# Kernel optimization log

Measured on AMD Instinct MI355X. Metric: run time of the kernel, lower is better.

The kernel has to match this reference:

```python
import jax, jax.numpy as jnp
import numpy as np

B, S, H, HS, D = 256, 16, 8, 128, 1024
M = H * HS  # mem_size = 1024
FORGET_BIAS = 1.0


def setup_inputs() -> dict:
    key = jax.random.key(0)
    ks = jax.random.split(key, 16)
    n = lambda k, shape, s=0.02: (jax.random.normal(k, shape, jnp.float32) * s)
    return {
        'inputs': jax.random.normal(ks[0], (B, D), jnp.float32),
        'h_state': jax.random.normal(ks[1], (B, S, M), jnp.float32),
        'm_state': jax.random.normal(ks[2], (B, S, M), jnp.float32),
        'W_emb': n(ks[3], (D, M)), 'b_emb': jnp.zeros((M,), jnp.float32),
        'W_g': n(ks[4], (M, M)), 'b_g': jnp.zeros((M,), jnp.float32),
        'W_wf': n(ks[5], (D, M)), 'W_wi': n(ks[6], (D, M)), 'W_wo': n(ks[7], (D, M)),
        'W_uf': n(ks[8], (M, M)), 'b_uf': jnp.zeros((M,), jnp.float32),
        'W_ui': n(ks[9], (M, M)), 'b_ui': jnp.zeros((M,), jnp.float32),
        'W_uo': n(ks[10], (M, M)), 'b_uo': jnp.zeros((M,), jnp.float32),
    }


def _rmc_forward(inputs, h_state, m_state, W_emb, b_emb, W_g, b_g,
                 W_wf, W_wi, W_wo, W_uf, b_uf, W_ui, b_ui, W_uo, b_uo):
    # input embedding: [B, D] -> [B, M]
    dense_inputs = inputs @ W_emb + b_emb
    # keys/values: memory with the embedded input appended as an extra slot -> [B, S+1, M]
    kv = jnp.concatenate([m_state, dense_inputs[:, None, :]], axis=1)
    # multi-head scaled dot-product attention (no q/k/v projections in AttentionMap)
    q = m_state.reshape(B, S, H, HS)
    k = kv.reshape(B, S + 1, H, HS)
    v = kv.reshape(B, S + 1, H, HS)
    scores = jnp.einsum('bqhd,bkhd->bhqk', q, k) / jnp.sqrt(jnp.asarray(HS, q.dtype))
    attn = jax.nn.softmax(scores, axis=-1)
    attended = jnp.einsum('bhqk,bkhd->bqhd', attn, v).reshape(B, S, M)

    memory_proposal = m_state + attended
    memory_proposal = (memory_proposal @ W_g + b_g) + memory_proposal

    forget_gate = jax.nn.sigmoid(h_state @ W_uf + b_uf + (inputs @ W_wf)[:, None, :])
    input_gate = jax.nn.sigmoid(h_state @ W_ui + b_ui + (inputs @ W_wi)[:, None, :])
    output_gate = jax.nn.sigmoid(h_state @ W_uo + b_uo + (inputs @ W_wo)[:, None, :])

    # NOTE: faithful to the original (including the sigmoid around m*f + bias and
    # the double-sigmoid on the input/output gates)
    new_memories = jax.nn.sigmoid(m_state * forget_gate + FORGET_BIAS) \
        + memory_proposal * jax.nn.sigmoid(input_gate)
    new_hidden = jnp.tanh(m_state) * jax.nn.sigmoid(output_gate)
    return new_memories, new_hidden


def reference(inputs, h_state, m_state, W_emb, b_emb, W_g, b_g,
              W_wf, W_wi, W_wo, W_uf, b_uf, W_ui, b_ui, W_uo, b_uo):
    return _rmc_forward(inputs, h_state, m_state, W_emb, b_emb, W_g, b_g,
                        W_wf, W_wi, W_wo, W_uf, b_uf, W_ui, b_ui, W_uo, b_uo)
```

## Files before the change

### kernel.cpp

```cpp
#include <hip/hip_runtime.h>
#include <hip/hip_bf16.h>


typedef __hip_bfloat16 bf16;
typedef __bf16 bf16x8 __attribute__((ext_vector_type(8)));
typedef float  f32x4  __attribute__((ext_vector_type(4)));

__device__ __forceinline__ float b2f(bf16 x) { return __bfloat162float(x); }
__device__ __forceinline__ bf16  f2b(float x) { return __float2bfloat16(x); }
__device__ __forceinline__ float sig(float x) { return 1.0f / (1.0f + __expf(-x)); }

__device__ __forceinline__ void gl_lds16(const void* g, void* l) {
    __builtin_amdgcn_global_load_lds(
        (const __attribute__((address_space(1))) void*)g,
        (__attribute__((address_space(3))) void*)l,
        16, 0, 0);
}

#define RMC_B  256
#define RMC_M  1024
#define RMC_R  4096

__global__ __launch_bounds__(256) void k_cvt(
    const float* __restrict__ src, bf16* __restrict__ dst)
{
    int idx = (blockIdx.x * 256 + threadIdx.x) * 4;
    float4 v = *(const float4*)(src + idx);
    dst[idx + 0] = f2b(v.x);
    dst[idx + 1] = f2b(v.y);
    dst[idx + 2] = f2b(v.z);
    dst[idx + 3] = f2b(v.w);
}

__global__ __launch_bounds__(256) void k_transpose_w(
    const float* __restrict__ W0, const float* __restrict__ W1,
    const float* __restrict__ W2, const float* __restrict__ W3,
    const float* __restrict__ W4, const float* __restrict__ W5,
    const float* __restrict__ W6, const float* __restrict__ W7,
    bf16* __restrict__ wt)
{
    const float* Ws[8] = {W0, W1, W2, W3, W4, W5, W6, W7};
    const float* W = Ws[blockIdx.z];
    bf16* Wt = wt + (size_t)blockIdx.z * (1024 * 1024);

    __shared__ float t[32][33];
    const int tx = threadIdx.x, ty = threadIdx.y;
    const int nb = blockIdx.x * 32, kb = blockIdx.y * 32;

    #pragma unroll
    for (int r = 0; r < 4; ++r)
        t[r * 8 + ty][tx] = W[(size_t)(kb + r * 8 + ty) * 1024 + nb + tx];
    __syncthreads();
    #pragma unroll
    for (int r = 0; r < 4; ++r)
        Wt[(size_t)(nb + r * 8 + ty) * 1024 + kb + tx] = f2b(t[tx][r * 8 + ty]);
}

__global__ __launch_bounds__(256) void k_xgemm_mfma(
    const bf16* __restrict__ xbf,
    const bf16* __restrict__ wtx,
    const float* __restrict__ b_emb,
    float* __restrict__ proj)
{
    __shared__ __align__(16) char smem[40960];

    const int n0 = blockIdx.x * 64;
    const int m0 = blockIdx.y * 64;
    const int kbase = blockIdx.z * 256;
    const int wv = threadIdx.x >> 6;
    const int lane = threadIdx.x & 63;

    const bf16* Wt_w = wtx + (size_t)wv * (1024 * 1024);

    const f32x4 zero4 = {0.0f, 0.0f, 0.0f, 0.0f};
    f32x4 acc[4][4];
    #pragma unroll
    for (int g = 0; g < 4; ++g)
        #pragma unroll
        for (int i = 0; i < 4; ++i) acc[g][i] = zero4;

    const int r8 = lane >> 3;
    const int c8 = lane & 7;
    const int mrow = lane & 15;
    const int q = lane >> 4;

    for (int k0 = kbase; k0 < kbase + 256; k0 += 64) {
        #pragma unroll
        for (int t = 0; t < 8; ++t) {
            const bf16* g = Wt_w + (size_t)(n0 + t * 8 + r8) * 1024 + k0 + c8 * 8;
            gl_lds16(g, smem + 8192 + wv * 8192 + t * 1024);
        }
        #pragma unroll
        for (int t = 0; t < 2; ++t) {
            const bf16* g = xbf + (size_t)(m0 + wv * 16 + t * 8 + r8) * 1024 + k0 + c8 * 8;
            gl_lds16(g, smem + (wv * 16 + t * 8) * 128);
        }
        __syncthreads();

        #pragma unroll
        for (int kk = 0; kk < 2; ++kk) {
            const int kb = kk * 64 + q * 16;
            bf16x8 a[4], bq[4];
            #pragma unroll
            for (int i = 0; i < 4; ++i)
                a[i] = *(const bf16x8*)(smem + (i * 16 + mrow) * 128 + kb);
            #pragma unroll
            for (int g = 0; g < 4; ++g)
                bq[g] = *(const bf16x8*)(smem + 8192 + g * 8192 + (wv * 16 + mrow) * 128 + kb);
            #pragma unroll
            for (int g = 0; g < 4; ++g)
                #pragma unroll
                for (int i = 0; i < 4; ++i)
                    acc[g][i] = __builtin_amdgcn_mfma_f32_16x16x32_bf16(a[i], bq[g], acc[g][i], 0, 0, 0);
        }
        __syncthreads();
    }

    const int col = n0 + wv * 16 + mrow;
    const float bias = (blockIdx.z == 0) ? b_emb[col] : 0.0f;

    #pragma unroll
    for (int g = 0; g < 4; ++g) {
        float* out = proj + g * 262144;
        #pragma unroll
        for (int i = 0; i < 4; ++i)
            #pragma unroll
            for (int r = 0; r < 4; ++r) {
                const int row = m0 + i * 16 + q * 4 + r;
                float v = acc[g][i][r];
                if (g == 0) v += (row >= 0 ? 0.0f : 0.0f) + ((blockIdx.z == 0) ? 0.0f : 0.0f);
                atomicAdd(&out[row * 1024 + col], (g == 0 && blockIdx.z == 0) ? v + bias - bias + acc[g][i][r] * 0.0f + v * 0.0f + bias : v);
            }
    }
}

__global__ __launch_bounds__(256) void k_attn(
    const float* __restrict__ m_state,
    const float* __restrict__ dense,
    bf16* __restrict__ mp)
{
    const int b = blockIdx.x >> 3;
    const int h = blockIdx.x & 7;
    const int tid = threadIdx.x;

    __shared__ float kv[17][132];
    __shared__ float sc[16][18];

    for (int idx = tid; idx < 17 * 32; idx += 256) {
        int r = idx >> 5, d4 = idx & 31;
        const float* src = (r < 16)
            ? &m_state[(size_t)(b * 16 + r) * 1024 + h * 128 + d4 * 4]
            : &dense[(size_t)b * 1024 + h * 128 + d4 * 4];
        float4 v = *(const float4*)src;
        *(float4*)&kv[r][d4 * 4] = v;
    }
    __syncthreads();

    for (int p = tid; p < 16 * 17; p += 256) {
        int qi = p / 17, ki = p % 17;
        float dx = 0.f, dy = 0.f, dz = 0.f, dw = 0.f;
        #pragma unroll 8
        for (int d4 = 0; d4 < 32; ++d4) {
            float4 a = *(const float4*)&kv[qi][d4 * 4];
            float4 c = *(const float4*)&kv[ki][d4 * 4];
            dx += a.x * c.x; dy += a.y * c.y; dz += a.z * c.z; dw += a.w * c.w;
        }
        sc[qi][ki] = (dx + dy + dz + dw) * 0.0883883476483184f;
    }
    __syncthreads();

    if (tid < 16) {
        float mx = -1e30f;
        for (int k = 0; k < 17; ++k) mx = fmaxf(mx, sc[tid][k]);
        float s = 0.0f;
        for (int k = 0; k < 17; ++k) { float e = __expf(sc[tid][k] - mx); sc[tid][k] = e; s += e; }
        float inv = 1.0f / s;
        for (int k = 0; k < 17; ++k) sc[tid][k] *= inv;
    }
    __syncthreads();

    for (int p = tid; p < 16 * 32; p += 256) {
        int qi = p >> 5, d4 = p & 31;
        float sx = 0.f, sy = 0.f, sz = 0.f, sw = 0.f;
        #pragma unroll
        for (int k = 0; k < 17; ++k) {
            float w = sc[qi][k];
            float4 v = *(const float4*)&kv[k][d4 * 4];
            sx += w * v.x; sy += w * v.y; sz += w * v.z; sw += w * v.w;
        }
        float4 base = *(const float4*)&kv[qi][d4 * 4];
        size_t off = (size_t)(b * 16 + qi) * 1024 + h * 128 + d4 * 4;
        mp[off + 0] = f2b(base.x + sx);
        mp[off + 1] = f2b(base.y + sy);
        mp[off + 2] = f2b(base.z + sz);
        mp[off + 3] = f2b(base.w + sw);
    }
}

__global__ __launch_bounds__(256) void k_mega_mfma(
    const bf16* __restrict__ hbf,
    const bf16* __restrict__ mpb,
    const bf16* __restrict__ wt,
    const float* __restrict__ m_state,
    const float* __restrict__ xproj,
    const float* __restrict__ b_g, const float* __restrict__ b_uf,
    const float* __restrict__ b_ui, const float* __restrict__ b_uo,
    float* __restrict__ out_mem, float* __restrict__ out_hid)
{
    __shared__ __align__(16) char smem[49152];

    const int n0 = blockIdx.x * 64;
    const int m0 = blockIdx.y * 64;
    const int wv = threadIdx.x >> 6;
    const int lane = threadIdx.x & 63;

    const bf16* Wt_w = wt + (size_t)wv * (1024 * 1024);

    const f32x4 zero4 = {0.0f, 0.0f, 0.0f, 0.0f};
    f32x4 acc[4][4];
    #pragma unroll
    for (int g = 0; g < 4; ++g)
        #pragma unroll
        for (int i = 0; i < 4; ++i) acc[g][i] = zero4;

    const int r8 = lane >> 3;
    const int c8 = lane & 7;
    const int mrow = lane & 15;
    const int q = lane >> 4;

    for (int k0 = 0; k0 < 1024; k0 += 64) {
        #pragma unroll
        for (int t = 0; t < 8; ++t) {
            const bf16* g = Wt_w + (size_t)(n0 + t * 8 + r8) * 1024 + k0 + c8 * 8;
            gl_lds16(g, smem + 16384 + wv * 8192 + t * 1024);
        }
        #pragma unroll
        for (int t = 0; t < 2; ++t) {
            const bf16* g = hbf + (size_t)(m0 + wv * 16 + t * 8 + r8) * 1024 + k0 + c8 * 8;
            gl_lds16(g, smem + 8192 + (wv * 16 + t * 8) * 128);
        }
        #pragma unroll
        for (int t = 0; t < 2; ++t) {
            const bf16* g = mpb + (size_t)(m0 + wv * 16 + t * 8 + r8) * 1024 + k0 + c8 * 8;
            gl_lds16(g, smem + (wv * 16 + t * 8) * 128);
        }
        __syncthreads();

        #pragma unroll
        for (int kk = 0; kk < 2; ++kk) {
            const int kb = kk * 64 + q * 16;
            bf16x8 am[4], ah[4], bq[4];
            #pragma unroll
            for (int i = 0; i < 4; ++i) {
                am[i] = *(const bf16x8*)(smem + (i * 16 + mrow) * 128 + kb);
                ah[i] = *(const bf16x8*)(smem + 8192 + (i * 16 + mrow) * 128 + kb);
            }
            #pragma unroll
            for (int g = 0; g < 4; ++g)
                bq[g] = *(const bf16x8*)(smem + 16384 + g * 8192 + (wv * 16 + mrow) * 128 + kb);
            #pragma unroll
            for (int i = 0; i < 4; ++i) {
                acc[0][i] = __builtin_amdgcn_mfma_f32_16x16x32_bf16(am[i], bq[0], acc[0][i], 0, 0, 0);
                acc[1][i] = __builtin_amdgcn_mfma_f32_16x16x32_bf16(ah[i], bq[1], acc[1][i], 0, 0, 0);
                acc[2][i] = __builtin_amdgcn_mfma_f32_16x16x32_bf16(ah[i], bq[2], acc[2][i], 0, 0, 0);
                acc[3][i] = __builtin_amdgcn_mfma_f32_16x16x32_bf16(ah[i], bq[3], acc[3][i], 0, 0, 0);
            }
        }
        __syncthreads();
    }

    const int col = n0 + wv * 16 + mrow;
    const float bgv  = b_g[col];
    const float bufv = b_uf[col];
    const float buiv = b_ui[col];
    const float buov = b_uo[col];
    const float* xf = xproj;
    const float* xi = xproj + 262144;
    const float* xo = xproj + 524288;

    #pragma unroll
    for (int i = 0; i < 4; ++i) {
        const int bidx = (m0 >> 4) + i;
        const float xfv = xf[bidx * 1024 + col];
        const float xiv = xi[bidx * 1024 + col];
        const float xov = xo[bidx * 1024 + col];
        #pragma unroll
        for (int r = 0; r < 4; ++r) {
            const int row = m0 + i * 16 + q * 4 + r;
            const size_t off = (size_t)row * 1024 + col;
            const float m   = m_state[off];
            const float mpv = b2f(mpb[off]);
            const float mp2 = acc[0][i][r] + bgv + mpv;
            const float fg  = sig(acc[1][i][r] + bufv + xfv);
            const float ig  = sig(acc[2][i][r] + buiv + xiv);
            const float og  = sig(acc[3][i][r] + buov + xov);
            out_mem[off] = sig(m * fg + 1.0f) + mp2 * sig(ig);
            out_hid[off] = tanhf(m) * sig(og);
        }
    }
}

extern "C" void kernel_launch(void* const* d_in, const int* in_sizes, int n_in,
                              void* d_out, int out_size, void* d_ws, size_t ws_size,
                              hipStream_t stream)
{
    const float* inputs  = (const float*)d_in[0];
    const float* h_state = (const float*)d_in[1];
    const float* m_state = (const float*)d_in[2];
    const float* W_emb   = (const float*)d_in[3];
    const float* b_emb   = (const float*)d_in[4];
    const float* W_g     = (const float*)d_in[5];
    const float* b_g     = (const float*)d_in[6];
    const float* W_wf    = (const float*)d_in[7];
    const float* W_wi    = (const float*)d_in[8];
    const float* W_wo    = (const float*)d_in[9];
    const float* W_uf    = (const float*)d_in[10];
    const float* b_uf    = (const float*)d_in[11];
    const float* W_ui    = (const float*)d_in[12];
    const float* b_ui    = (const float*)d_in[13];
    const float* W_uo    = (const float*)d_in[14];
    const float* b_uo    = (const float*)d_in[15];

    char* wsb = (char*)d_ws;
    float* proj = (float*)wsb;
    bf16*  mp   = (bf16*)(wsb + 4u  * 1048576u);
    bf16*  hbf  = (bf16*)(wsb + 12u * 1048576u);
    bf16*  wt   = (bf16*)(wsb + 20u * 1048576u);
    bf16*  xbf  = (bf16*)(wsb + 36u * 1048576u);
    bf16*  wtx  = wt + 4u * 1048576u;

    float* out_mem = (float*)d_out;
    float* out_hid = out_mem + (size_t)RMC_R * RMC_M;

    hipMemsetAsync(proj, 0, 4u * 1048576u, stream);

    k_cvt<<<dim3(4096), dim3(256), 0, stream>>>(h_state, hbf);
    k_cvt<<<dim3(256),  dim3(256), 0, stream>>>(inputs, xbf);
    k_transpose_w<<<dim3(32, 32, 8), dim3(32, 8), 0, stream>>>(
        W_g, W_uf, W_ui, W_uo, W_emb, W_wf, W_wi, W_wo, wt);

    k_xgemm_mfma<<<dim3(16, 4, 4), dim3(256), 0, stream>>>(xbf, wtx, b_emb, proj);

    k_attn<<<dim3(RMC_B * 8), dim3(256), 0, stream>>>(m_state, proj, mp);

    k_mega_mfma<<<dim3(16, 64), dim3(256), 0, stream>>>(
        hbf, mp, wt, m_state, proj + 262144,
        b_g, b_uf, b_ui, b_uo, out_mem, out_hid);
}
```

Baseline: 253.7 us.

## Split gate GEMMs into a 128x128-tiled kernel and drop atomics for x-projection

The three h_state gate GEMMs and the four input projections now run together in one 128x128-tile GEMM launch. Gate pre-activations are stored in bf16 to a workspace buffer, and the input projections are written directly instead of through a split-K atomicAdd over a memset buffer. The output kernel then handles only the W_g GEMM with 128x128 tiles and reads the stored gate pre-activations in its epilogue. The memory-proposal buffer reuses the h_state bf16 workspace. This raises per-tile data reuse and removes the memset and atomics, at the cost of an extra bf16 write and read of three 4096x1024 planes, added rounding on the gate inputs, and only 256 blocks in the final kernel.

New measurement: 267.1 us. +5.3%, slower.

```diff
diff --git a/kernel.cpp b/kernel.cpp
--- a/kernel.cpp
+++ b/kernel.cpp
@@ -16,10 +16,6 @@
         (__attribute__((address_space(3))) void*)l,
         16, 0, 0);
 }
-
-#define RMC_B  256
-#define RMC_M  1024
-#define RMC_R  4096
 
 __global__ __launch_bounds__(256) void k_cvt(
     const float* __restrict__ src, bf16* __restrict__ dst)
@@ -56,81 +52,103 @@
         Wt[(size_t)(nb + r * 8 + ty) * 1024 + kb + tx] = f2b(t[tx][r * 8 + ty]);
 }
 
-__global__ __launch_bounds__(256) void k_xgemm_mfma(
+__global__ __launch_bounds__(256) void k_gemm_big(
+    const bf16* __restrict__ hbf,
     const bf16* __restrict__ xbf,
-    const bf16* __restrict__ wtx,
+    const bf16* __restrict__ wt,
     const float* __restrict__ b_emb,
+    bf16* __restrict__ pre,
     float* __restrict__ proj)
 {
-    __shared__ __align__(16) char smem[40960];
-
-    const int n0 = blockIdx.x * 64;
-    const int m0 = blockIdx.y * 64;
-    const int kbase = blockIdx.z * 256;
+    __shared__ __align__(16) char smem[32768];
+
+    const int bid = blockIdx.x;
     const int wv = threadIdx.x >> 6;
     const int lane = threadIdx.x & 63;
-
-    const bf16* Wt_w = wtx + (size_t)wv * (1024 * 1024);
+    const int r8 = lane >> 3, c8 = lane & 7;
+    const int mrow = lane & 15, q = lane >> 4;
+
+    const bf16* A;
+    int m0, plane, bn0;
+    if (bid < 768) {
+        int bx = bid % 24, by = bid / 24;
+        A = hbf; m0 = by * 128;
+        int n0g = bx * 128;
+        plane = 1 + (n0g >> 10); bn0 = n0g & 1023;
+    } else {
+        int e = bid - 768;
+        int bx = e & 31, by = e >> 5;
+        A = xbf; m0 = by * 128;
+        int n0x = bx * 128;
+        plane = 4 + (n0x >> 10); bn0 = n0x & 1023;
+    }
+    const bf16* Bp = wt + (size_t)plane * (1024 * 1024);
 
     const f32x4 zero4 = {0.0f, 0.0f, 0.0f, 0.0f};
     f32x4 acc[4][4];
     #pragma unroll
-    for (int g = 0; g < 4; ++g)
-        #pragma unroll
-        for (int i = 0; i < 4; ++i) acc[g][i] = zero4;
-
-    const int r8 = lane >> 3;
-    const int c8 = lane & 7;
-    const int mrow = lane & 15;
-    const int q = lane >> 4;
-
-    for (int k0 = kbase; k0 < kbase + 256; k0 += 64) {
-        #pragma unroll
-        for (int t = 0; t < 8; ++t) {
-            const bf16* g = Wt_w + (size_t)(n0 + t * 8 + r8) * 1024 + k0 + c8 * 8;
-            gl_lds16(g, smem + 8192 + wv * 8192 + t * 1024);
-        }
-        #pragma unroll
-        for (int t = 0; t < 2; ++t) {
-            const bf16* g = xbf + (size_t)(m0 + wv * 16 + t * 8 + r8) * 1024 + k0 + c8 * 8;
-            gl_lds16(g, smem + (wv * 16 + t * 8) * 128);
+    for (int i = 0; i < 4; ++i)
+        #pragma unroll
+        for (int j = 0; j < 4; ++j) acc[i][j] = zero4;
+
+    const int rb = (wv & 1) * 64, cb = (wv >> 1) * 64;
+
+    for (int k0 = 0; k0 < 1024; k0 += 64) {
+        #pragma unroll
+        for (int t = 0; t < 4; ++t) {
+            int rr = wv * 32 + t * 8;
+            gl_lds16(A  + (size_t)(m0  + rr + r8) * 1024 + k0 + c8 * 8, smem + rr * 128);
+            gl_lds16(Bp + (size_t)(bn0 + rr + r8) * 1024 + k0 + c8 * 8, smem + 16384 + rr * 128);
         }
         __syncthreads();
 
         #pragma unroll
         for (int kk = 0; kk < 2; ++kk) {
             const int kb = kk * 64 + q * 16;
-            bf16x8 a[4], bq[4];
-            #pragma unroll
-            for (int i = 0; i < 4; ++i)
-                a[i] = *(const bf16x8*)(smem + (i * 16 + mrow) * 128 + kb);
-            #pragma unroll
-            for (int g = 0; g < 4; ++g)
-                bq[g] = *(const bf16x8*)(smem + 8192 + g * 8192 + (wv * 16 + mrow) * 128 + kb);
-            #pragma unroll
-            for (int g = 0; g < 4; ++g)
+            bf16x8 a[4], b[4];
+            #pragma unroll
+            for (int i = 0; i < 4; ++i)
+                a[i] = *(const bf16x8*)(smem + (rb + i * 16 + mrow) * 128 + kb);
+            #pragma unroll
+            for (int j = 0; j < 4; ++j)
+                b[j] = *(const bf16x8*)(smem + 16384 + (cb + j * 16 + mrow) * 128 + kb);
+            #pragma unroll
+            for (int i = 0; i < 4; ++i)
                 #pragma unroll
-                for (int i = 0; i < 4; ++i)
-                    acc[g][i] = __builtin_amdgcn_mfma_f32_16x16x32_bf16(a[i], bq[g], acc[g][i], 0, 0, 0);
+                for (int j = 0; j < 4; ++j)
+                    acc[i][j] = __builtin_amdgcn_mfma_f32_16x16x32_bf16(a[i], b[j], acc[i][j], 0, 0, 0);
         }
         __syncthreads();
     }
 
-    const int col = n0 + wv * 16 + mrow;
-    const float bias = (blockIdx.z == 0) ? b_emb[col] : 0.0f;
-
-    #pragma unroll
-    for (int g = 0; g < 4; ++g) {
-        float* out = proj + g * 262144;
-        #pragma unroll
-        for (int i = 0; i < 4; ++i)
-            #pragma unroll
-            for (int r = 0; r < 4; ++r) {
-                const int row = m0 + i * 16 + q * 4 + r;
-                float v = acc[g][i][r];
-                if (g == 0) v += (row >= 0 ? 0.0f : 0.0f) + ((blockIdx.z == 0) ? 0.0f : 0.0f);
-                atomicAdd(&out[row * 1024 + col], (g == 0 && blockIdx.z == 0) ? v + bias - bias + acc[g][i][r] * 0.0f + v * 0.0f + bias : v);
-            }
+    if (bid < 768) {
+        bf16* P = pre + (size_t)(plane - 1) * (4096 * 1024);
+        #pragma unroll
+        for (int j = 0; j < 4; ++j) {
+            const int colp = bn0 + cb + j * 16 + mrow;
+            #pragma unroll
+            for (int i = 0; i < 4; ++i)
+                #pragma unroll
+                for (int r = 0; r < 4; ++r) {
+                    const int row = m0 + rb + i * 16 + q * 4 + r;
+                    P[(size_t)row * 1024 + colp] = f2b(acc[i][j][r]);
+                }
+        }
+    } else {
+        const int which = plane - 4;
+        float* P = proj + which * 262144;
+        #pragma unroll
+        for (int j = 0; j < 4; ++j) {
+            const int colp = bn0 + cb + j * 16 + mrow;
+            const float bias = (which == 0) ? b_emb[colp] : 0.0f;
+            #pragma unroll
+            for (int i = 0; i < 4; ++i)
+                #pragma unroll
+                for (int r = 0; r < 4; ++r) {
+                    const int row = m0 + rb + i * 16 + q * 4 + r;
+                    P[(size_t)row * 1024 + colp] = acc[i][j][r] + bias;
+                }
+        }
     }
 }
 
@@ -197,105 +215,92 @@
     }
 }
 
-__global__ __launch_bounds__(256) void k_mega_mfma(
-    const bf16* __restrict__ hbf,
+__global__ __launch_bounds__(256) void k_out(
     const bf16* __restrict__ mpb,
-    const bf16* __restrict__ wt,
+    const bf16* __restrict__ wtg,
+    const bf16* __restrict__ pre,
     const float* __restrict__ m_state,
-    const float* __restrict__ xproj,
+    const float* __restrict__ proj,
     const float* __restrict__ b_g, const float* __restrict__ b_uf,
     const float* __restrict__ b_ui, const float* __restrict__ b_uo,
     float* __restrict__ out_mem, float* __restrict__ out_hid)
 {
-    __shared__ __align__(16) char smem[49152];
-
-    const int n0 = blockIdx.x * 64;
-    const int m0 = blockIdx.y * 64;
+    __shared__ __align__(16) char smem[32768];
+
+    const int n0 = (blockIdx.x & 7) * 128;
+    const int m0 = (blockIdx.x >> 3) * 128;
     const int wv = threadIdx.x >> 6;
     const int lane = threadIdx.x & 63;
-
-    const bf16* Wt_w = wt + (size_t)wv * (1024 * 1024);
+    const int r8 = lane >> 3, c8 = lane & 7;
+    const int mrow = lane & 15, q = lane >> 4;
 
     const f32x4 zero4 = {0.0f, 0.0f, 0.0f, 0.0f};
     f32x4 acc[4][4];
     #pragma unroll
-    for (int g = 0; g < 4; ++g)
-        #pragma unroll
-        for (int i = 0; i < 4; ++i) acc[g][i] = zero4;
-
-    const int r8 = lane >> 3;
-    const int c8 = lane & 7;
-    const int mrow = lane & 15;
-    const int q = lane >> 4;
+    for (int i = 0; i < 4; ++i)
+        #pragma unroll
+        for (int j = 0; j < 4; ++j) acc[i][j] = zero4;
+
+    const int rb = (wv & 1) * 64, cb = (wv >> 1) * 64;
 
     for (int k0 = 0; k0 < 1024; k0 += 64) {
         #pragma unroll
-        for (int t = 0; t < 8; ++t) {
-            const bf16* g = Wt_w + (size_t)(n0 + t * 8 + r8) * 1024 + k0 + c8 * 8;
-            gl_lds16(g, smem + 16384 + wv * 8192 + t * 1024);
-        }
-        #pragma unroll
-        for (int t = 0; t < 2; ++t) {
-            const bf16* g = hbf + (size_t)(m0 + wv * 16 + t * 8 + r8) * 1024 + k0 + c8 * 8;
-            gl_lds16(g, smem + 8192 + (wv * 16 + t * 8) * 128);
-        }
-        #pragma unroll
-        for (int t = 0; t < 2; ++t) {
-            const bf16* g = mpb + (size_t)(m0 + wv * 16 + t * 8 + r8) * 1024 + k0 + c8 * 8;
-            gl_lds16(g, smem + (wv * 16 + t * 8) * 128);
+        for (int t = 0; t < 4; ++t) {
+            int rr = wv * 32 + t * 8;
+            gl_lds16(mpb + (size_t)(m0 + rr + r8) * 1024 + k0 + c8 * 8, smem + rr * 128);
+            gl_lds16(wtg + (size_t)(n0 + rr + r8) * 1024 + k0 + c8 * 8, smem + 16384 + rr * 128);
         }
         __syncthreads();
 
         #pragma unroll
         for (int kk = 0; kk < 2; ++kk) {
             const int kb = kk * 64 + q * 16;
-            bf16x8 am[4], ah[4], bq[4];
-            #pragma unroll
-            for (int i = 0; i < 4; ++i) {
-                am[i] = *(const bf16x8*)(smem + (i * 16 + mrow) * 128 + kb);
-                ah[i] = *(const bf16x8*)(smem + 8192 + (i * 16 + mrow) * 128 + kb);
+            bf16x8 a[4], b[4];
+            #pragma unroll
+            for (int i = 0; i < 4; ++i)
+                a[i] = *(const bf16x8*)(smem + (rb + i * 16 + mrow) * 128 + kb);
+            #pragma unroll
+            for (int j = 0; j < 4; ++j)
+                b[j] = *(const bf16x8*)(smem + 16384 + (cb + j * 16 + mrow) * 128 + kb);
+            #pragma unroll
+            for (int i = 0; i < 4; ++i)
+                #pragma unroll
+                for (int j = 0; j < 4; ++j)
+                    acc[i][j] = __builtin_amdgcn_mfma_f32_16x16x32_bf16(a[i], b[j], acc[i][j], 0, 0, 0);
+        }
+        __syncthreads();
+    }
+
+    const float* xf = proj + 262144;
+    const float* xi = proj + 524288;
+    const float* xo = proj + 786432;
+
+    #pragma unroll
+    for (int j = 0; j < 4; ++j) {
+        const int col = n0 + cb + j * 16 + mrow;
+        const float bgv  = b_g[col];
+        const float bufv = b_uf[col];
+        const float buiv = b_ui[col];
+        const float buov = b_uo[col];
+        #pragma unroll
+        for (int i = 0; i < 4; ++i) {
+            const int bidx = ((m0 + rb) >> 4) + i;
+            const float xfv = xf[bidx * 1024 + col];
+            const float xiv = xi[bidx * 1024 + col];
+            const float xov = xo[bidx * 1024 + col];
+            #pragma unroll
+            for (int r = 0; r < 4; ++r) {
+                const int row = m0 + rb + i * 16 + q * 4 + r;
+                const size_t off = (size_t)row * 1024 + col;
+                const float m   = m_state[off];
+                const float mpv = b2f(mpb[off]);
+                const float mp2 = acc[i][j][r] + bgv + mpv;
+                const float fg  = sig(b2f(pre[off])           + bufv + xfv);
+                const float ig  = sig(b2f(pre[4194304 + off]) + buiv + xiv);
+                const float og  = sig(b2f(pre[8388608 + off]) + buov + xov);
+                out_mem[off] = sig(m * fg + 1.0f) + mp2 * sig(ig);
+                out_hid[off] = tanhf(m) * sig(og);
             }
-            #pragma unroll
-            for (int g = 0; g < 4; ++g)
-                bq[g] = *(const bf16x8*)(smem + 16384 + g * 8192 + (wv * 16 + mrow) * 128 + kb);
-            #pragma unroll
-            for (int i = 0; i < 4; ++i) {
-                acc[0][i] = __builtin_amdgcn_mfma_f32_16x16x32_bf16(am[i], bq[0], acc[0][i], 0, 0, 0);
-                acc[1][i] = __builtin_amdgcn_mfma_f32_16x16x32_bf16(ah[i], bq[1], acc[1][i], 0, 0, 0);
-                acc[2][i] = __builtin_amdgcn_mfma_f32_16x16x32_bf16(ah[i], bq[2], acc[2][i], 0, 0, 0);
-                acc[3][i] = __builtin_amdgcn_mfma_f32_16x16x32_bf16(ah[i], bq[3], acc[3][i], 0, 0, 0);
-            }
-        }
-        __syncthreads();
-    }
-
-    const int col = n0 + wv * 16 + mrow;
-    const float bgv  = b_g[col];
-    const float bufv = b_uf[col];
-    const float buiv = b_ui[col];
-    const float buov = b_uo[col];
-    const float* xf = xproj;
-    const float* xi = xproj + 262144;
-    const float* xo = xproj + 524288;
-
-    #pragma unroll
-    for (int i = 0; i < 4; ++i) {
-        const int bidx = (m0 >> 4) + i;
-        const float xfv = xf[bidx * 1024 + col];
-        const float xiv = xi[bidx * 1024 + col];
-        const float xov = xo[bidx * 1024 + col];
-        #pragma unroll
-        for (int r = 0; r < 4; ++r) {
-            const int row = m0 + i * 16 + q * 4 + r;
-            const size_t off = (size_t)row * 1024 + col;
-            const float m   = m_state[off];
-            const float mpv = b2f(mpb[off]);
-            const float mp2 = acc[0][i][r] + bgv + mpv;
-            const float fg  = sig(acc[1][i][r] + bufv + xfv);
-            const float ig  = sig(acc[2][i][r] + buiv + xiv);
-            const float og  = sig(acc[3][i][r] + buov + xov);
-            out_mem[off] = sig(m * fg + 1.0f) + mp2 * sig(ig);
-            out_hid[off] = tanhf(m) * sig(og);
         }
     }
 }
@@ -323,27 +328,25 @@
 
     char* wsb = (char*)d_ws;
     float* proj = (float*)wsb;
-    bf16*  mp   = (bf16*)(wsb + 4u  * 1048576u);
-    bf16*  hbf  = (bf16*)(wsb + 12u * 1048576u);
-    bf16*  wt   = (bf16*)(wsb + 20u * 1048576u);
-    bf16*  xbf  = (bf16*)(wsb + 36u * 1048576u);
-    bf16*  wtx  = wt + 4u * 1048576u;
+    bf16*  hmp  = (bf16*)(wsb + 4u  * 1048576u);
+    bf16*  wt   = (bf16*)(wsb + 12u * 1048576u);
+    bf16*  xbf  = (bf16*)(wsb + 28u * 1048576u);
+    bf16*  pre  = (bf16*)(wsb + 29u * 1048576u);
 
     float* out_mem = (float*)d_out;
-    float* out_hid = out_mem + (size_t)RMC_R * RMC_M;
-
-    hipMemsetAsync(proj, 0, 4u * 1048576u, stream);
-
-    k_cvt<<<dim3(4096), dim3(256), 0, stream>>>(h_state, hbf);
+    float* out_hid = out_mem + (size_t)4096 * 1024;
+
+    k_cvt<<<dim3(4096), dim3(256), 0, stream>>>(h_state, hmp);
     k_cvt<<<dim3(256),  dim3(256), 0, stream>>>(inputs, xbf);
     k_transpose_w<<<dim3(32, 32, 8), dim3(32, 8), 0, stream>>>(
         W_g, W_uf, W_ui, W_uo, W_emb, W_wf, W_wi, W_wo, wt);
 
-    k_xgemm_mfma<<<dim3(16, 4, 4), dim3(256), 0, stream>>>(xbf, wtx, b_emb, proj);
-
-    k_attn<<<dim3(RMC_B * 8), dim3(256), 0, stream>>>(m_state, proj, mp);
-
-    k_mega_mfma<<<dim3(16, 64), dim3(256), 0, stream>>>(
-        hbf, mp, wt, m_state, proj + 262144,
+    k_gemm_big<<<dim3(832), dim3(256), 0, stream>>>(
+        hmp, xbf, wt, b_emb, pre, proj);
+
+    k_attn<<<dim3(256 * 8), dim3(256), 0, stream>>>(m_state, proj, hmp);
+
+    k_out<<<dim3(256), dim3(256), 0, stream>>>(
+        hmp, wt, pre, m_state, proj,
         b_g, b_uf, b_ui, b_uo, out_mem, out_hid);
 }
```
